# Optimization experiments

Hardware: AMD Instinct MI355X
Metric: run time of the kernel (lower is better)

The kernel has to match this reference:

```python
import jax, jax.numpy as jnp
import numpy as np

N = 100000   # nodes
E = 600000   # edges
IN = 12      # in_dim
H = 128      # hidden_dim
OUT = 2      # out_dim
L = 3        # num_layers
EPS = 1e-5   # BatchNorm eps


def setup_inputs() -> dict:
    key = jax.random.key(0)
    ks = jax.random.split(key, 14)
    s = 0.05
    return {
        "features": jax.random.normal(ks[0], (N, IN), jnp.float32),
        "edge_index": jax.random.randint(ks[1], (2, E), 0, N, dtype=jnp.int32).astype(jnp.int64),
        "emb_W": jax.random.normal(ks[2], (IN, H), jnp.float32) * s,
        "emb_b": jnp.zeros((H,), jnp.float32),
        "Wself": jax.random.normal(ks[3], (L, H, H), jnp.float32) * s,
        "Wneigh": jax.random.normal(ks[4], (L, H, H), jnp.float32) * s,
        "conv_b": jnp.zeros((L, H), jnp.float32),
        "bn_gamma": jnp.ones((L, H), jnp.float32),
        "bn_beta": jnp.zeros((L, H), jnp.float32),
        "W1": jax.random.normal(ks[5], (H, H // 2), jnp.float32) * s,
        "b1": jnp.zeros((H // 2,), jnp.float32),
        "W2": jax.random.normal(ks[6], (H // 2, OUT), jnp.float32) * s,
        "b2": jnp.zeros((OUT,), jnp.float32),
    }


def reference(features, edge_index, emb_W, emb_b, Wself, Wneigh, conv_b,
              bn_gamma, bn_beta, W1, b1, W2, b2):
    src, dst = edge_index[0], edge_index[1]
    # in-degree per destination node (loop-invariant)
    deg = jax.ops.segment_sum(jnp.ones((E,), features.dtype), dst, num_segments=N)
    inv_deg = 1.0 / jnp.maximum(deg, 1.0)  # [N]

    h = features @ emb_W + emb_b           # embedding: [N, H]
    h_last = h
    for i in range(L):
        # SAGEConv 'mean': gather src feats, scatter-sum to dst, divide by degree
        msg_sum = jax.ops.segment_sum(h[src], dst, num_segments=N)  # [N, H]
        h_neigh = msg_sum * inv_deg[:, None]
        h_new = h @ Wself[i] + h_neigh @ Wneigh[i] + conv_b[i]
        # BatchNorm1d over nodes (batch statistics)
        mu = jnp.mean(h_new, axis=0)
        var = jnp.var(h_new, axis=0)
        h_new = (h_new - mu) * jax.lax.rsqrt(var + EPS) * bn_gamma[i] + bn_beta[i]
        h_new = jax.nn.relu(h_new)
        # dropout is identity at inference
        if i > 0:
            h_new = h_new + h_last  # residual
        h_last = h_new
        h = h_new
    # MLP head
    out = jax.nn.relu(h @ W1 + b1) @ W2 + b2  # [N, 2]
    return out
```

## Files before the change

kernel.cpp:

```cpp
#include <hip/hip_runtime.h>
#include <hip/hip_bf16.h>
#include <cstdint>

#define H 128
#define EPS 1e-5f
#define CAP 32
#define NB 16

typedef unsigned int uint;
typedef unsigned short ushort;
typedef short short8 __attribute__((ext_vector_type(8)));
typedef float f32x4 __attribute__((ext_vector_type(4)));

__device__ __forceinline__ ushort f2bf(float f) {
  uint u = __float_as_uint(f);
  u += 0x7fffu + ((u >> 16) & 1u);
  return (ushort)(u >> 16);
}
__device__ __forceinline__ float bflo(uint v) { return __uint_as_float(v << 16); }
__device__ __forceinline__ float bfhi(uint v) { return __uint_as_float(v & 0xffff0000u); }

__global__ __launch_bounds__(256) void k_init(const void* __restrict__ ei, int N,
                                              uint* __restrict__ cnt, int* __restrict__ flag,
                                              const float* __restrict__ F, const float* __restrict__ embW,
                                              const float* __restrict__ embB,
                                              ushort* __restrict__ bufA, ushort* __restrict__ bufB,
                                              const float* __restrict__ Wself, const float* __restrict__ Wneigh,
                                              const float* __restrict__ W1,
                                              ushort* __restrict__ Wsw, ushort* __restrict__ W1sw,
                                              float* __restrict__ bn_all,
                                              int ZB, int EB) {
  __shared__ float sW[12 * 128];
  __shared__ float sF[256 * 12];
  int b = blockIdx.x, t = threadIdx.x;
  if (b < ZB) {
    int i = b * 256 + t;
    if (i < N) cnt[i] = 0u;
    if (b == 0) {
      for (int j = t; j < NB * 256 * 3; j += 256) bn_all[j] = 0.f;
      if (t == 0) {
        const long long* p = (const long long*)ei;
        int ok = 1;
        for (int j = 0; j < 16; ++j) {
          long long s = p[j];
          if (s < 0 || s >= (long long)N) ok = 0;
        }
        *flag = ok;
      }
    }
    return;
  }
  if (b < ZB + EB) {
    int blk = b - ZB;
    for (int i = t; i < 12 * 128; i += 256) sW[i] = embW[i];
    int row0 = blk * 256;
    int nrows = min(256, N - row0);
    for (int i = t; i < nrows * 12; i += 256) sF[i] = F[(size_t)row0 * 12 + i];
    __syncthreads();
    int col = t & 127, half = t >> 7;
    float bias = embB[col];
    int rlo = half * 128, rhi = min(nrows, rlo + 128);
    for (int r = rlo; r < rhi; ++r) {
      float acc = bias;
#pragma unroll
      for (int k = 0; k < 12; ++k) acc = fmaf(sF[r * 12 + k], sW[k * 128 + col], acc);
      bufA[(size_t)(row0 + r) * H + col] = f2bf(acc);
    }
    if (blk == 0 && t < 128) {
      bufA[(size_t)N * H + t] = 0;
      bufB[(size_t)N * H + t] = 0;
    }
    return;
  }
  int e = (b - ZB - EB) * 256 + t;
  if (e < 3 * 4096) {
    int l = e >> 12, r = e & 4095;
    int kt = r >> 9, nt = (r >> 6) & 7, lane = r & 63;
    int quad = lane >> 4, l16 = lane & 15;
    int n = nt * 16 + l16;
    ushort* dst = Wsw + ((size_t)l * 4096 + (kt * 8 + nt) * 64 + lane) * 8;
#pragma unroll
    for (int j = 0; j < 8; ++j) {
      int k = kt * 32 + quad * 8 + j;
      float v = (k < 128) ? Wself[(size_t)l * H * H + (size_t)k * H + n]
                          : Wneigh[(size_t)l * H * H + (size_t)(k - 128) * H + n];
      dst[j] = f2bf(v);
    }
  } else if (e < 3 * 4096 + 1024) {
    int r = e - 3 * 4096;
    int kt = r >> 8, nt = (r >> 6) & 3, lane = r & 63;
    int quad = lane >> 4, l16 = lane & 15;
    int n = nt * 16 + l16;
    ushort* dst = W1sw + ((size_t)((kt * 4 + nt) * 64 + lane)) * 8;
#pragma unroll
    for (int j = 0; j < 8; ++j) {
      int k = kt * 32 + quad * 8 + j;
      dst[j] = f2bf(W1[(size_t)k * 64 + n]);
    }
  }
}

__global__ __launch_bounds__(256) void k_fill(const void* __restrict__ ei, uint* __restrict__ cnt,
                                              uint* __restrict__ csr, int E,
                                              const int* __restrict__ flag) {
  int e0 = (blockIdx.x * 256 + threadIdx.x) * 2;
  if (e0 >= E) return;
  int is64 = *flag;
  int s0, s1 = -1, d0, d1 = -1;
  bool two = (e0 + 1 < E);
  if (is64) {
    const unsigned long long* p = (const unsigned long long*)ei;
    if (two) {
      ulong2 sv = *(const ulong2*)(p + e0);
      ulong2 dv = *(const ulong2*)(p + E + e0);
      s0 = (int)sv.x; s1 = (int)sv.y; d0 = (int)dv.x; d1 = (int)dv.y;
    } else {
      s0 = (int)p[e0]; d0 = (int)p[E + e0];
    }
  } else {
    const int* p = (const int*)ei;
    if (two) {
      int2 sv = *(const int2*)(p + e0);
      int2 dv = *(const int2*)(p + E + e0);
      s0 = sv.x; s1 = sv.y; d0 = dv.x; d1 = dv.y;
    } else {
      s0 = p[e0]; d0 = p[E + e0];
    }
  }
  uint p0 = atomicAdd(&cnt[d0], 1u);
  if (p0 < (uint)CAP) csr[(size_t)d0 * CAP + p0] = (uint)s0;
  if (two) {
    uint p1 = atomicAdd(&cnt[d1], 1u);
    if (p1 < (uint)CAP) csr[(size_t)d1 * CAP + p1] = (uint)s1;
  }
}

__global__ __launch_bounds__(256, 4) void k_gg(const ushort* __restrict__ h, ushort* __restrict__ z,
                                               const uint* __restrict__ cnt, const uint* __restrict__ csr,
                                               const ushort* __restrict__ Wsw, const float* __restrict__ bias,
                                               float* __restrict__ bn_acc, int N) {
  __shared__ ushort sMsg[128 * 128];
  int tid = threadIdx.x;
  int wave = tid >> 6, lane = tid & 63, quad = lane >> 4, l16 = lane & 15;
  int row0 = blockIdx.x * 128;

  {
    const uint4* hu = (const uint4*)h;
#pragma unroll
    for (int p = 0; p < 8; ++p) {
      int nl = p * 16 + wave * 4 + quad;
      int n = row0 + nl;
      uint rawc = (n < N) ? cnt[n] : 0u;
      uint deg = min(rawc, (uint)CAP);
      const uint* row = csr + (size_t)n * CAP;
      float a0 = 0.f, a1 = 0.f, a2 = 0.f, a3 = 0.f, a4 = 0.f, a5 = 0.f, a6 = 0.f, a7 = 0.f;
      for (uint k = 0; k < deg; k += 8) {
        uint4 r0 = *(const uint4*)(row + k);
        uint4 r1 = *(const uint4*)(row + k + 4);
        uint raw[8] = {r0.x, r0.y, r0.z, r0.w, r1.x, r1.y, r1.z, r1.w};
        uint idx[8];
#pragma unroll
        for (int j = 0; j < 8; ++j) idx[j] = (k + j < deg) ? raw[j] : (uint)N;
        uint4 v[8];
#pragma unroll
        for (int j = 0; j < 8; ++j) v[j] = hu[(size_t)idx[j] * 16 + l16];
#pragma unroll
        for (int j = 0; j < 8; ++j) {
          a0 += bflo(v[j].x); a1 += bfhi(v[j].x);
          a2 += bflo(v[j].y); a3 += bfhi(v[j].y);
          a4 += bflo(v[j].z); a5 += bfhi(v[j].z);
          a6 += bflo(v[j].w); a7 += bfhi(v[j].w);
        }
      }
      float inv = 1.0f / (float)max(rawc, 1u);
      uint4 o;
      o.x = (uint)f2bf(a0 * inv) | ((uint)f2bf(a1 * inv) << 16);
      o.y = (uint)f2bf(a2 * inv) | ((uint)f2bf(a3 * inv) << 16);
      o.z = (uint)f2bf(a4 * inv) | ((uint)f2bf(a5 * inv) << 16);
      o.w = (uint)f2bf(a6 * inv) | ((uint)f2bf(a7 * inv) << 16);
      int off = nl * 256 + ((l16 * 16) ^ ((nl & 7) << 4));
      *(uint4*)((char*)sMsg + off) = o;
    }
  }

  int wrow0 = row0 + wave * 32;
  f32x4 acc[2][8];
#pragma unroll
  for (int m = 0; m < 2; ++m)
#pragma unroll
    for (int nt = 0; nt < 8; ++nt) acc[m][nt] = (f32x4){0.f, 0.f, 0.f, 0.f};
  short8 zf8 = {0, 0, 0, 0, 0, 0, 0, 0};
  const short8* Bp = (const short8*)Wsw;

#pragma unroll
  for (int kt = 0; kt < 4; ++kt) {
    int colb = kt * 32 + quad * 8;
    short8 a[2];
#pragma unroll
    for (int m = 0; m < 2; ++m) {
      int row = wrow0 + m * 16 + l16;
      a[m] = (row < N) ? *(const short8*)(h + (size_t)row * H + colb) : zf8;
    }
#pragma unroll
    for (int nt = 0; nt < 8; ++nt) {
      short8 bfr = Bp[(kt * 8 + nt) * 64 + lane];
#pragma unroll
      for (int m = 0; m < 2; ++m)
        acc[m][nt] = __builtin_amdgcn_mfma_f32_16x16x32_bf16(a[m], bfr, acc[m][nt], 0, 0, 0);
    }
  }
  __syncthreads();
#pragma unroll
  for (int kt = 4; kt < 8; ++kt) {
    int cb = (kt - 4) * 64 + quad * 16;
    short8 a[2];
#pragma unroll
    for (int m = 0; m < 2; ++m) {
      int rl = wave * 32 + m * 16 + l16;
      a[m] = *(const short8*)((const char*)sMsg + rl * 256 + (cb ^ ((l16 & 7) << 4)));
    }
#pragma unroll
    for (int nt = 0; nt < 8; ++nt) {
      short8 bfr = Bp[(kt * 8 + nt) * 64 + lane];
#pragma unroll
      for (int m = 0; m < 2; ++m)
        acc[m][nt] = __builtin_amdgcn_mfma_f32_16x16x32_bf16(a[m], bfr, acc[m][nt], 0, 0, 0);
    }
  }

  float bs[8];
#pragma unroll
  for (int nt = 0; nt < 8; ++nt) bs[nt] = bias[nt * 16 + l16];
  float ps[8], pq[8];
#pragma unroll
  for (int nt = 0; nt < 8; ++nt) { ps[nt] = 0.f; pq[nt] = 0.f; }
#pragma unroll
  for (int m = 0; m < 2; ++m) {
#pragma unroll
    for (int nt = 0; nt < 8; ++nt) {
      int col = nt * 16 + l16;
#pragma unroll
      for (int r = 0; r < 4; ++r) {
        int row = wrow0 + m * 16 + quad * 4 + r;
        if (row < N) {
          float v = acc[m][nt][r] + bs[nt];
          z[(size_t)row * H + col] = f2bf(v);
          ps[nt] += v; pq[nt] += v * v;
        }
      }
    }
  }
  __syncthreads();
  float* red = (float*)sMsg;
  int wq = wave * 4 + quad;
#pragma unroll
  for (int nt = 0; nt < 8; ++nt) {
    red[(wq * 8 + nt) * 17 + l16] = ps[nt];
    red[2176 + (wq * 8 + nt) * 17 + l16] = pq[nt];
  }
  __syncthreads();
  if (tid < 128) {
    int nt = tid >> 4, lc = tid & 15;
    float s = 0.f, q = 0.f;
#pragma unroll
    for (int w2i = 0; w2i < 16; ++w2i) {
      s += red[(w2i * 8 + nt) * 17 + lc];
      q += red[2176 + (w2i * 8 + nt) * 17 + lc];
    }
    float* bank = bn_acc + (size_t)(blockIdx.x & (NB - 1)) * 256;
    atomicAdd(&bank[tid], s);
    atomicAdd(&bank[128 + tid], q);
  }
}

__global__ __launch_bounds__(256) void k_norm(uint4* __restrict__ z, const uint4* __restrict__ hprev,
                                              const float* __restrict__ bn_acc,
                                              const float* __restrict__ gamma,
                                              const float* __restrict__ beta,
                                              int residual, int n4, float invN) {
  __shared__ float ssc[128], ssh[128];
  int t = threadIdx.x;
  if (t < 128) {
    float s = 0.f, q = 0.f;
#pragma unroll
    for (int b = 0; b < NB; ++b) {
      s += bn_acc[b * 256 + t];
      q += bn_acc[b * 256 + 128 + t];
    }
    float mu = s * invN;
    float var = fmaxf(q * invN - mu * mu, 0.f);
    float sc = gamma[t] * rsqrtf(var + EPS);
    ssc[t] = sc;
    ssh[t] = beta[t] - mu * sc;
  }
  __syncthreads();
  int idx = blockIdx.x * 256 + t;
  if (idx >= n4) return;
  int j = (idx & 15) * 8;
  uint4 v = z[idx];
  float x0 = fmaxf(fmaf(bflo(v.x), ssc[j + 0], ssh[j + 0]), 0.f);
  float x1 = fmaxf(fmaf(bfhi(v.x), ssc[j + 1], ssh[j + 1]), 0.f);
  float x2 = fmaxf(fmaf(bflo(v.y), ssc[j + 2], ssh[j + 2]), 0.f);
  float x3 = fmaxf(fmaf(bfhi(v.y), ssc[j + 3], ssh[j + 3]), 0.f);
  float x4 = fmaxf(fmaf(bflo(v.z), ssc[j + 4], ssh[j + 4]), 0.f);
  float x5 = fmaxf(fmaf(bfhi(v.z), ssc[j + 5], ssh[j + 5]), 0.f);
  float x6 = fmaxf(fmaf(bflo(v.w), ssc[j + 6], ssh[j + 6]), 0.f);
  float x7 = fmaxf(fmaf(bfhi(v.w), ssc[j + 7], ssh[j + 7]), 0.f);
  if (residual) {
    uint4 r = hprev[idx];
    x0 += bflo(r.x); x1 += bfhi(r.x); x2 += bflo(r.y); x3 += bfhi(r.y);
    x4 += bflo(r.z); x5 += bfhi(r.z); x6 += bflo(r.w); x7 += bfhi(r.w);
  }
  uint4 o;
  o.x = (uint)f2bf(x0) | ((uint)f2bf(x1) << 16);
  o.y = (uint)f2bf(x2) | ((uint)f2bf(x3) << 16);
  o.z = (uint)f2bf(x4) | ((uint)f2bf(x5) << 16);
  o.w = (uint)f2bf(x6) | ((uint)f2bf(x7) << 16);
  z[idx] = o;
}

__global__ __launch_bounds__(256) void k_head(const ushort* __restrict__ z, const ushort* __restrict__ hprev,
                                              const float* __restrict__ bn_acc,
                                              const float* __restrict__ gamma,
                                              const float* __restrict__ beta, float invN,
                                              const ushort* __restrict__ W1sw,
                                              const float* __restrict__ b1, const float* __restrict__ W2,
                                              const float* __restrict__ b2, float* __restrict__ out, int N) {
  __shared__ float ssc[128], ssh[128];
  int tid = threadIdx.x;
  if (tid < 128) {
    float s = 0.f, q = 0.f;
#pragma unroll
    for (int b = 0; b < NB; ++b) {
      s += bn_acc[b * 256 + tid];
      q += bn_acc[b * 256 + 128 + tid];
    }
    float mu = s * invN;
    float var = fmaxf(q * invN - mu * mu, 0.f);
    float sc = gamma[tid] * rsqrtf(var + EPS);
    ssc[tid] = sc;
    ssh[tid] = beta[tid] - mu * sc;
  }
  __syncthreads();
  int wave = tid >> 6, lane = tid & 63, quad = lane >> 4, l16 = lane & 15;
  int wrow0 = blockIdx.x * 64 + wave * 16;
  int am = wrow0 + l16;
  bool avalid = am < N;
  short8 af[4];
#pragma unroll
  for (int kt = 0; kt < 4; ++kt) {
    int c0 = kt * 32 + quad * 8;
    uint4 vz = avalid ? ((const uint4*)z)[(size_t)am * 16 + kt * 4 + quad] : make_uint4(0, 0, 0, 0);
    uint4 vr = avalid ? ((const uint4*)hprev)[(size_t)am * 16 + kt * 4 + quad] : make_uint4(0, 0, 0, 0);
    float x0 = fmaxf(fmaf(bflo(vz.x), ssc[c0 + 0], ssh[c0 + 0]), 0.f) + bflo(vr.x);
    float x1 = fmaxf(fmaf(bfhi(vz.x), ssc[c0 + 1], ssh[c0 + 1]), 0.f) + bfhi(vr.x);
    float x2 = fmaxf(fmaf(bflo(vz.y), ssc[c0 + 2], ssh[c0 + 2]), 0.f) + bflo(vr.y);
    float x3 = fmaxf(fmaf(bfhi(vz.y), ssc[c0 + 3], ssh[c0 + 3]), 0.f) + bfhi(vr.y);
    float x4 = fmaxf(fmaf(bflo(vz.z), ssc[c0 + 4], ssh[c0 + 4]), 0.f) + bflo(vr.z);
    float x5 = fmaxf(fmaf(bfhi(vz.z), ssc[c0 + 5], ssh[c0 + 5]), 0.f) + bfhi(vr.z);
    float x6 = fmaxf(fmaf(bflo(vz.w), ssc[c0 + 6], ssh[c0 + 6]), 0.f) + bflo(vr.w);
    float x7 = fmaxf(fmaf(bfhi(vz.w), ssc[c0 + 7], ssh[c0 + 7]), 0.f) + bfhi(vr.w);
    ushort u[8] = {f2bf(x0), f2bf(x1), f2bf(x2), f2bf(x3), f2bf(x4), f2bf(x5), f2bf(x6), f2bf(x7)};
    af[kt] = *(short8*)u;
  }
  const short8* Bp = (const short8*)W1sw;
  f32x4 acc[4];
#pragma unroll
  for (int nt = 0; nt < 4; ++nt) acc[nt] = (f32x4){0.f, 0.f, 0.f, 0.f};
#pragma unroll
  for (int kt = 0; kt < 4; ++kt) {
#pragma unroll
    for (int nt = 0; nt < 4; ++nt) {
      short8 bfr = Bp[(kt * 4 + nt) * 64 + lane];
      acc[nt] = __builtin_amdgcn_mfma_f32_16x16x32_bf16(af[kt], bfr, acc[nt], 0, 0, 0);
    }
  }
  float p0[4] = {0.f, 0.f, 0.f, 0.f}, p1[4] = {0.f, 0.f, 0.f, 0.f};
#pragma unroll
  for (int nt = 0; nt < 4; ++nt) {
    int c = nt * 16 + l16;
    float bc = b1[c], w20 = W2[c * 2], w21 = W2[c * 2 + 1];
#pragma unroll
    for (int r = 0; r < 4; ++r) {
      float v = fmaxf(acc[nt][r] + bc, 0.f);
      p0[r] = fmaf(v, w20, p0[r]);
      p1[r] = fmaf(v, w21, p1[r]);
    }
  }
#pragma unroll
  for (int m = 1; m < 16; m <<= 1) {
#pragma unroll
    for (int r = 0; r < 4; ++r) {
      p0[r] += __shfl_xor(p0[r], m);
      p1[r] += __shfl_xor(p1[r], m);
    }
  }
  if (l16 == 0) {
    float b20 = b2[0], b21 = b2[1];
#pragma unroll
    for (int r = 0; r < 4; ++r) {
      int row = wrow0 + quad * 4 + r;
      if (row < N) {
        float2 o = make_float2(p0[r] + b20, p1[r] + b21);
        *(float2*)(out + (size_t)row * 2) = o;
      }
    }
  }
}

extern "C" void kernel_launch(void* const* d_in, const int* in_sizes, int n_in,
                              void* d_out, int out_size, void* d_ws, size_t ws_size,
                              hipStream_t stream) {
  const float* features = (const float*)d_in[0];
  const void*  edges    = d_in[1];
  const float* emb_W    = (const float*)d_in[2];
  const float* emb_b    = (const float*)d_in[3];
  const float* Wself    = (const float*)d_in[4];
  const float* Wneigh   = (const float*)d_in[5];
  const float* conv_b   = (const float*)d_in[6];
  const float* bn_gamma = (const float*)d_in[7];
  const float* bn_beta  = (const float*)d_in[8];
  const float* W1       = (const float*)d_in[9];
  const float* b1       = (const float*)d_in[10];
  const float* W2       = (const float*)d_in[11];
  const float* b2       = (const float*)d_in[12];
  float* out = (float*)d_out;
  const int N = in_sizes[0] / 12;
  const int E = in_sizes[1] / 2;
  const float invN = 1.0f / (float)N;

  char* ws = (char*)d_ws;
  size_t off = 0;
  auto take = [&](size_t bytes) {
    char* p = ws + off;
    off = (off + bytes + 511) & ~(size_t)511;
    return p;
  };
  int*    flag   = (int*)take(4);
  uint*   cnt    = (uint*)take((size_t)N * 4);
  uint*   csr    = (uint*)take((size_t)N * CAP * 4);
  float*  bn_all = (float*)take(NB * 256 * 3 * 4);
  ushort* Wsw    = (ushort*)take(3 * 4096 * 8 * 2);
  ushort* W1sw   = (ushort*)take(1024 * 8 * 2);
  ushort* bufA   = (ushort*)take(((size_t)N + 1) * H * 2);
  ushort* bufB   = (ushort*)take(((size_t)N + 1) * H * 2);

  const int ZB = (N + 255) / 256;
  const int EB = (N + 255) / 256;
  const int PB = (3 * 4096 + 1024 + 255) / 256;
  const int FB = (E + 511) / 512;
  const int GB = (N + 127) / 128;

  k_init<<<ZB + EB + PB, 256, 0, stream>>>(edges, N, cnt, flag, features, emb_W, emb_b,
                                           bufA, bufB, Wself, Wneigh, W1, Wsw, W1sw, bn_all, ZB, EB);
  k_fill<<<FB, 256, 0, stream>>>(edges, cnt, csr, E, flag);

  ushort* hbuf = bufA;
  ushort* obuf = bufB;
  const int n4 = N * 16;
  for (int i = 0; i < 3; ++i) {
    float* bn_i = bn_all + (size_t)i * NB * 256;
    k_gg<<<GB, 256, 0, stream>>>(hbuf, obuf, cnt, csr, Wsw + (size_t)i * 4096 * 8,
                                 conv_b + (size_t)i * H, bn_i, N);
    if (i < 2) {
      k_norm<<<(n4 + 255) / 256, 256, 0, stream>>>((uint4*)obuf, (const uint4*)hbuf, bn_i,
                                                   bn_gamma + (size_t)i * H, bn_beta + (size_t)i * H,
                                                   (i > 0) ? 1 : 0, n4, invN);
      ushort* t = hbuf; hbuf = obuf; obuf = t;
    }
  }
  k_head<<<(N + 63) / 64, 256, 0, stream>>>(obuf, hbuf, bn_all + (size_t)2 * NB * 256,
                                            bn_gamma + 2 * H, bn_beta + 2 * H,
                                            invN, W1sw, b1, W2, b2, out, N);
}
```

Baseline: 309.7 us.

## Fuse layer-0 BatchNorm+ReLU into layer-1 gather-GEMM and merge norm passes

Removes the standalone normalization pass after layer 0. The layer-1 gather/GEMM kernel now applies the layer-0 BN scale/shift and ReLU on the fly, both to gathered neighbor rows (with a mask for padding) and to the self rows. A combined k_norm2 later writes normalized layer-1 output plus the normalized layer-0 residual. This saves one full read/write pass over the N×128 activation, at the cost of extra ALU work per gathered element inside the bandwidth-bound gather loop.

Result: no change. 308.7 us (-0.3%).

```diff
diff --git a/kernel.cpp b/kernel.cpp
--- a/kernel.cpp
+++ b/kernel.cpp
@@ -19,6 +19,9 @@
 }
 __device__ __forceinline__ float bflo(uint v) { return __uint_as_float(v << 16); }
 __device__ __forceinline__ float bfhi(uint v) { return __uint_as_float(v & 0xffff0000u); }
+__device__ __forceinline__ float nrm(float x, float sc, float sh) {
+  return fmaxf(fmaf(x, sc, sh), 0.f);
+}
 
 __global__ __launch_bounds__(256) void k_init(const void* __restrict__ ei, int N,
                                               uint* __restrict__ cnt, int* __restrict__ flag,
@@ -135,14 +138,41 @@
   }
 }
 
+template <int MODE>
 __global__ __launch_bounds__(256, 4) void k_gg(const ushort* __restrict__ h, ushort* __restrict__ z,
                                                const uint* __restrict__ cnt, const uint* __restrict__ csr,
                                                const ushort* __restrict__ Wsw, const float* __restrict__ bias,
-                                               float* __restrict__ bn_acc, int N) {
+                                               float* __restrict__ bn_acc, int N,
+                                               const float* __restrict__ bn_prev,
+                                               const float* __restrict__ gprev,
+                                               const float* __restrict__ bprev, float invN) {
   __shared__ ushort sMsg[128 * 128];
+  __shared__ float ssc[128], ssh[128];
   int tid = threadIdx.x;
   int wave = tid >> 6, lane = tid & 63, quad = lane >> 4, l16 = lane & 15;
   int row0 = blockIdx.x * 128;
+
+  if (MODE) {
+    if (tid < 128) {
+      float s = 0.f, q = 0.f;
+#pragma unroll
+      for (int b = 0; b < NB; ++b) {
+        s += bn_prev[b * 256 + tid];
+        q += bn_prev[b * 256 + 128 + tid];
+      }
+      float mu = s * invN;
+      float var = fmaxf(q * invN - mu * mu, 0.f);
+      float sc = gprev[tid] * rsqrtf(var + EPS);
+      ssc[tid] = sc;
+      ssh[tid] = bprev[tid] - mu * sc;
+    }
+    __syncthreads();
+  }
+  float sc8[8], sh8[8];
+  if (MODE) {
+#pragma unroll
+    for (int e = 0; e < 8; ++e) { sc8[e] = ssc[l16 * 8 + e]; sh8[e] = ssh[l16 * 8 + e]; }
+  }
 
   {
     const uint4* hu = (const uint4*)h;
@@ -159,17 +189,33 @@
         uint4 r1 = *(const uint4*)(row + k + 4);
         uint raw[8] = {r0.x, r0.y, r0.z, r0.w, r1.x, r1.y, r1.z, r1.w};
         uint idx[8];
-#pragma unroll
-        for (int j = 0; j < 8; ++j) idx[j] = (k + j < deg) ? raw[j] : (uint)N;
+        float msk[8];
+#pragma unroll
+        for (int j = 0; j < 8; ++j) {
+          bool in = (k + j < deg);
+          idx[j] = in ? raw[j] : (uint)N;
+          msk[j] = in ? 1.f : 0.f;
+        }
         uint4 v[8];
 #pragma unroll
         for (int j = 0; j < 8; ++j) v[j] = hu[(size_t)idx[j] * 16 + l16];
 #pragma unroll
         for (int j = 0; j < 8; ++j) {
-          a0 += bflo(v[j].x); a1 += bfhi(v[j].x);
-          a2 += bflo(v[j].y); a3 += bfhi(v[j].y);
-          a4 += bflo(v[j].z); a5 += bfhi(v[j].z);
-          a6 += bflo(v[j].w); a7 += bfhi(v[j].w);
+          if (MODE) {
+            a0 = fmaf(nrm(bflo(v[j].x), sc8[0], sh8[0]), msk[j], a0);
+            a1 = fmaf(nrm(bfhi(v[j].x), sc8[1], sh8[1]), msk[j], a1);
+            a2 = fmaf(nrm(bflo(v[j].y), sc8[2], sh8[2]), msk[j], a2);
+            a3 = fmaf(nrm(bfhi(v[j].y), sc8[3], sh8[3]), msk[j], a3);
+            a4 = fmaf(nrm(bflo(v[j].z), sc8[4], sh8[4]), msk[j], a4);
+            a5 = fmaf(nrm(bfhi(v[j].z), sc8[5], sh8[5]), msk[j], a5);
+            a6 = fmaf(nrm(bflo(v[j].w), sc8[6], sh8[6]), msk[j], a6);
+            a7 = fmaf(nrm(bfhi(v[j].w), sc8[7], sh8[7]), msk[j], a7);
+          } else {
+            a0 += bflo(v[j].x); a1 += bfhi(v[j].x);
+            a2 += bflo(v[j].y); a3 += bfhi(v[j].y);
+            a4 += bflo(v[j].z); a5 += bfhi(v[j].z);
+            a6 += bflo(v[j].w); a7 += bfhi(v[j].w);
+          }
         }
       }
       float inv = 1.0f / (float)max(rawc, 1u);
@@ -195,11 +241,34 @@
 #pragma unroll
   for (int kt = 0; kt < 4; ++kt) {
     int colb = kt * 32 + quad * 8;
+    float scv[8], shv[8];
+    if (MODE) {
+#pragma unroll
+      for (int e = 0; e < 8; ++e) { scv[e] = ssc[colb + e]; shv[e] = ssh[colb + e]; }
+    }
     short8 a[2];
 #pragma unroll
     for (int m = 0; m < 2; ++m) {
       int row = wrow0 + m * 16 + l16;
-      a[m] = (row < N) ? *(const short8*)(h + (size_t)row * H + colb) : zf8;
+      if (row < N) {
+        if (MODE) {
+          uint4 vz = *(const uint4*)(h + (size_t)row * H + colb);
+          ushort u[8];
+          u[0] = f2bf(nrm(bflo(vz.x), scv[0], shv[0]));
+          u[1] = f2bf(nrm(bfhi(vz.x), scv[1], shv[1]));
+          u[2] = f2bf(nrm(bflo(vz.y), scv[2], shv[2]));
+          u[3] = f2bf(nrm(bfhi(vz.y), scv[3], shv[3]));
+          u[4] = f2bf(nrm(bflo(vz.z), scv[4], shv[4]));
+          u[5] = f2bf(nrm(bfhi(vz.z), scv[5], shv[5]));
+          u[6] = f2bf(nrm(bflo(vz.w), scv[6], shv[6]));
+          u[7] = f2bf(nrm(bfhi(vz.w), scv[7], shv[7]));
+          a[m] = *(short8*)u;
+        } else {
+          a[m] = *(const short8*)(h + (size_t)row * H + colb);
+        }
+      } else {
+        a[m] = zf8;
+      }
     }
 #pragma unroll
     for (int nt = 0; nt < 8; ++nt) {
@@ -273,50 +342,50 @@
   }
 }
 
-__global__ __launch_bounds__(256) void k_norm(uint4* __restrict__ z, const uint4* __restrict__ hprev,
-                                              const float* __restrict__ bn_acc,
-                                              const float* __restrict__ gamma,
-                                              const float* __restrict__ beta,
-                                              int residual, int n4, float invN) {
-  __shared__ float ssc[128], ssh[128];
+__global__ __launch_bounds__(256) void k_norm2(const uint4* __restrict__ z1, uint4* __restrict__ zh,
+                                               const float* __restrict__ bn1, const float* __restrict__ g1v,
+                                               const float* __restrict__ b1v,
+                                               const float* __restrict__ bn0, const float* __restrict__ g0v,
+                                               const float* __restrict__ b0v,
+                                               int n4, float invN) {
+  __shared__ float s1c[128], s1h[128], s0c[128], s0h[128];
   int t = threadIdx.x;
   if (t < 128) {
     float s = 0.f, q = 0.f;
 #pragma unroll
-    for (int b = 0; b < NB; ++b) {
-      s += bn_acc[b * 256 + t];
-      q += bn_acc[b * 256 + 128 + t];
-    }
+    for (int b = 0; b < NB; ++b) { s += bn1[b * 256 + t]; q += bn1[b * 256 + 128 + t]; }
     float mu = s * invN;
     float var = fmaxf(q * invN - mu * mu, 0.f);
-    float sc = gamma[t] * rsqrtf(var + EPS);
-    ssc[t] = sc;
-    ssh[t] = beta[t] - mu * sc;
+    float sc = g1v[t] * rsqrtf(var + EPS);
+    s1c[t] = sc; s1h[t] = b1v[t] - mu * sc;
+    s = 0.f; q = 0.f;
+#pragma unroll
+    for (int b = 0; b < NB; ++b) { s += bn0[b * 256 + t]; q += bn0[b * 256 + 128 + t]; }
+    mu = s * invN;
+    var = fmaxf(q * invN - mu * mu, 0.f);
+    sc = g0v[t] * rsqrtf(var + EPS);
+    s0c[t] = sc; s0h[t] = b0v[t] - mu * sc;
   }
   __syncthreads();
   int idx = blockIdx.x * 256 + t;
   if (idx >= n4) return;
   int j = (idx & 15) * 8;
-  uint4 v = z[idx];
-  float x0 = fmaxf(fmaf(bflo(v.x), ssc[j + 0], ssh[j + 0]), 0.f);
-  float x1 = fmaxf(fmaf(bfhi(v.x), ssc[j + 1], ssh[j + 1]), 0.f);
-  float x2 = fmaxf(fmaf(bflo(v.y), ssc[j + 2], ssh[j + 2]), 0.f);
-  float x3 = fmaxf(fmaf(bfhi(v.y), ssc[j + 3], ssh[j + 3]), 0.f);
-  float x4 = fmaxf(fmaf(bflo(v.z), ssc[j + 4], ssh[j + 4]), 0.f);
-  float x5 = fmaxf(fmaf(bfhi(v.z), ssc[j + 5], ssh[j + 5]), 0.f);
-  float x6 = fmaxf(fmaf(bflo(v.w), ssc[j + 6], ssh[j + 6]), 0.f);
-  float x7 = fmaxf(fmaf(bfhi(v.w), ssc[j + 7], ssh[j + 7]), 0.f);
-  if (residual) {
-    uint4 r = hprev[idx];
-    x0 += bflo(r.x); x1 += bfhi(r.x); x2 += bflo(r.y); x3 += bfhi(r.y);
-    x4 += bflo(r.z); x5 += bfhi(r.z); x6 += bflo(r.w); x7 += bfhi(r.w);
-  }
+  uint4 v = z1[idx];
+  uint4 r = zh[idx];
+  float x0 = nrm(bflo(v.x), s1c[j + 0], s1h[j + 0]) + nrm(bflo(r.x), s0c[j + 0], s0h[j + 0]);
+  float x1 = nrm(bfhi(v.x), s1c[j + 1], s1h[j + 1]) + nrm(bfhi(r.x), s0c[j + 1], s0h[j + 1]);
+  float x2 = nrm(bflo(v.y), s1c[j + 2], s1h[j + 2]) + nrm(bflo(r.y), s0c[j + 2], s0h[j + 2]);
+  float x3 = nrm(bfhi(v.y), s1c[j + 3], s1h[j + 3]) + nrm(bfhi(r.y), s0c[j + 3], s0h[j + 3]);
+  float x4 = nrm(bflo(v.z), s1c[j + 4], s1h[j + 4]) + nrm(bflo(r.z), s0c[j + 4], s0h[j + 4]);
+  float x5 = nrm(bfhi(v.z), s1c[j + 5], s1h[j + 5]) + nrm(bfhi(r.z), s0c[j + 5], s0h[j + 5]);
+  float x6 = nrm(bflo(v.w), s1c[j + 6], s1h[j + 6]) + nrm(bflo(r.w), s0c[j + 6], s0h[j + 6]);
+  float x7 = nrm(bfhi(v.w), s1c[j + 7], s1h[j + 7]) + nrm(bfhi(r.w), s0c[j + 7], s0h[j + 7]);
   uint4 o;
   o.x = (uint)f2bf(x0) | ((uint)f2bf(x1) << 16);
   o.y = (uint)f2bf(x2) | ((uint)f2bf(x3) << 16);
   o.z = (uint)f2bf(x4) | ((uint)f2bf(x5) << 16);
   o.w = (uint)f2bf(x6) | ((uint)f2bf(x7) << 16);
-  z[idx] = o;
+  zh[idx] = o;
 }
 
 __global__ __launch_bounds__(256) void k_head(const ushort* __restrict__ z, const ushort* __restrict__ hprev,
@@ -352,14 +421,14 @@
     int c0 = kt * 32 + quad * 8;
     uint4 vz = avalid ? ((const uint4*)z)[(size_t)am * 16 + kt * 4 + quad] : make_uint4(0, 0, 0, 0);
     uint4 vr = avalid ? ((const uint4*)hprev)[(size_t)am * 16 + kt * 4 + quad] : make_uint4(0, 0, 0, 0);
-    float x0 = fmaxf(fmaf(bflo(vz.x), ssc[c0 + 0], ssh[c0 + 0]), 0.f) + bflo(vr.x);
-    float x1 = fmaxf(fmaf(bfhi(vz.x), ssc[c0 + 1], ssh[c0 + 1]), 0.f) + bfhi(vr.x);
-    float x2 = fmaxf(fmaf(bflo(vz.y), ssc[c0 + 2], ssh[c0 + 2]), 0.f) + bflo(vr.y);
-    float x3 = fmaxf(fmaf(bfhi(vz.y), ssc[c0 + 3], ssh[c0 + 3]), 0.f) + bfhi(vr.y);
-    float x4 = fmaxf(fmaf(bflo(vz.z), ssc[c0 + 4], ssh[c0 + 4]), 0.f) + bflo(vr.z);
-    float x5 = fmaxf(fmaf(bfhi(vz.z), ssc[c0 + 5], ssh[c0 + 5]), 0.f) + bfhi(vr.z);
-    float x6 = fmaxf(fmaf(bflo(vz.w), ssc[c0 + 6], ssh[c0 + 6]), 0.f) + bflo(vr.w);
-    float x7 = fmaxf(fmaf(bfhi(vz.w), ssc[c0 + 7], ssh[c0 + 7]), 0.f) + bfhi(vr.w);
+    float x0 = nrm(bflo(vz.x), ssc[c0 + 0], ssh[c0 + 0]) + bflo(vr.x);
+    float x1 = nrm(bfhi(vz.x), ssc[c0 + 1], ssh[c0 + 1]) + bfhi(vr.x);
+    float x2 = nrm(bflo(vz.y), ssc[c0 + 2], ssh[c0 + 2]) + bflo(vr.y);
+    float x3 = nrm(bfhi(vz.y), ssc[c0 + 3], ssh[c0 + 3]) + bfhi(vr.y);
+    float x4 = nrm(bflo(vz.z), ssc[c0 + 4], ssh[c0 + 4]) + bflo(vr.z);
+    float x5 = nrm(bfhi(vz.z), ssc[c0 + 5], ssh[c0 + 5]) + bfhi(vr.z);
+    float x6 = nrm(bflo(vz.w), ssc[c0 + 6], ssh[c0 + 6]) + bflo(vr.w);
+    float x7 = nrm(bfhi(vz.w), ssc[c0 + 7], ssh[c0 + 7]) + bfhi(vr.w);
     ushort u[8] = {f2bf(x0), f2bf(x1), f2bf(x2), f2bf(x3), f2bf(x4), f2bf(x5), f2bf(x6), f2bf(x7)};
     af[kt] = *(short8*)u;
   }
@@ -455,21 +524,20 @@
                                            bufA, bufB, Wself, Wneigh, W1, Wsw, W1sw, bn_all, ZB, EB);
   k_fill<<<FB, 256, 0, stream>>>(edges, cnt, csr, E, flag);
 
-  ushort* hbuf = bufA;
-  ushort* obuf = bufB;
+  float* bn0 = bn_all;
+  float* bn1 = bn_all + (size_t)NB * 256;
+  float* bn2 = bn_all + (size_t)2 * NB * 256;
   const int n4 = N * 16;
-  for (int i = 0; i < 3; ++i) {
-    float* bn_i = bn_all + (size_t)i * NB * 256;
-    k_gg<<<GB, 256, 0, stream>>>(hbuf, obuf, cnt, csr, Wsw + (size_t)i * 4096 * 8,
-                                 conv_b + (size_t)i * H, bn_i, N);
-    if (i < 2) {
-      k_norm<<<(n4 + 255) / 256, 256, 0, stream>>>((uint4*)obuf, (const uint4*)hbuf, bn_i,
-                                                   bn_gamma + (size_t)i * H, bn_beta + (size_t)i * H,
-                                                   (i > 0) ? 1 : 0, n4, invN);
-      ushort* t = hbuf; hbuf = obuf; obuf = t;
-    }
-  }
-  k_head<<<(N + 63) / 64, 256, 0, stream>>>(obuf, hbuf, bn_all + (size_t)2 * NB * 256,
-                                            bn_gamma + 2 * H, bn_beta + 2 * H,
+
+  k_gg<0><<<GB, 256, 0, stream>>>(bufA, bufB, cnt, csr, Wsw, conv_b, bn0, N,
+                                  nullptr, nullptr, nullptr, invN);
+  k_gg<1><<<GB, 256, 0, stream>>>(bufB, bufA, cnt, csr, Wsw + (size_t)4096 * 8, conv_b + H, bn1, N,
+                                  bn0, bn_gamma, bn_beta, invN);
+  k_norm2<<<(n4 + 255) / 256, 256, 0, stream>>>((const uint4*)bufA, (uint4*)bufB,
+                                                bn1, bn_gamma + H, bn_beta + H,
+                                                bn0, bn_gamma, bn_beta, n4, invN);
+  k_gg<0><<<GB, 256, 0, stream>>>(bufB, bufA, cnt, csr, Wsw + (size_t)2 * 4096 * 8, conv_b + 2 * H,
+                                  bn2, N, nullptr, nullptr, nullptr, invN);
+  k_head<<<(N + 63) / 64, 256, 0, stream>>>(bufA, bufB, bn2, bn_gamma + 2 * H, bn_beta + 2 * H,
                                             invN, W1sw, b1, W2, b2, out, N);
 }
```

## Fuse BatchNorm apply into layer kernel via grid barrier, merge CSR fill

Applied to the files above, without the earlier changes.

For layers 0 and 1, the conv/GEMM kernel now keeps its pre-norm results in registers. It waits at a grid-wide atomic barrier until all blocks have contributed batch statistics, then computes scale and shift and writes the normalized ReLU (plus residual) output directly. This removes two separate normalize passes over the N×128 bf16 activations and their launches. Separately, the zero-init work moves into its own small kernel so the edge CSR fill can share one launch with the embedding and weight packing. The barrier relies on all blocks being co-resident, so it is only used when the grid has at most 1024 blocks; blocks spin-wait while stragglers finish.

Measured after the change: 650.6 us. 2.1x slower.

```diff
diff --git a/kernel.cpp b/kernel.cpp
--- a/kernel.cpp
+++ b/kernel.cpp
@@ -19,39 +19,82 @@
 }
 __device__ __forceinline__ float bflo(uint v) { return __uint_as_float(v << 16); }
 __device__ __forceinline__ float bfhi(uint v) { return __uint_as_float(v & 0xffff0000u); }
-
-__global__ __launch_bounds__(256) void k_init(const void* __restrict__ ei, int N,
+__device__ __forceinline__ float nrm(float x, float sc, float sh) {
+  return fmaxf(fmaf(x, sc, sh), 0.f);
+}
+
+__global__ __launch_bounds__(256) void k_zero(const void* __restrict__ ei, int N,
                                               uint* __restrict__ cnt, int* __restrict__ flag,
+                                              float* __restrict__ bn_all, uint* __restrict__ bar,
+                                              ushort* __restrict__ bufA, ushort* __restrict__ bufB) {
+  int b = blockIdx.x, t = threadIdx.x;
+  int i = b * 256 + t;
+  if (i < N) cnt[i] = 0u;
+  if (b == 0) {
+    for (int j = t; j < NB * 256 * 3; j += 256) bn_all[j] = 0.f;
+    if (t < 2) bar[t] = 0u;
+    if (t < 128) {
+      bufA[(size_t)N * H + t] = 0;
+      bufB[(size_t)N * H + t] = 0;
+    }
+    if (t == 0) {
+      const long long* p = (const long long*)ei;
+      int ok = 1;
+      for (int j = 0; j < 16; ++j) {
+        long long s = p[j];
+        if (s < 0 || s >= (long long)N) ok = 0;
+      }
+      *flag = ok;
+    }
+  }
+}
+
+__global__ __launch_bounds__(256) void k_work(const void* __restrict__ ei, uint* __restrict__ cnt,
+                                              uint* __restrict__ csr, int E, const int* __restrict__ flag,
                                               const float* __restrict__ F, const float* __restrict__ embW,
-                                              const float* __restrict__ embB,
-                                              ushort* __restrict__ bufA, ushort* __restrict__ bufB,
+                                              const float* __restrict__ embB, ushort* __restrict__ bufA,
                                               const float* __restrict__ Wself, const float* __restrict__ Wneigh,
                                               const float* __restrict__ W1,
                                               ushort* __restrict__ Wsw, ushort* __restrict__ W1sw,
-                                              float* __restrict__ bn_all,
-                                              int ZB, int EB) {
+                                              int N, int FB, int EB) {
   __shared__ float sW[12 * 128];
   __shared__ float sF[256 * 12];
   int b = blockIdx.x, t = threadIdx.x;
-  if (b < ZB) {
-    int i = b * 256 + t;
-    if (i < N) cnt[i] = 0u;
-    if (b == 0) {
-      for (int j = t; j < NB * 256 * 3; j += 256) bn_all[j] = 0.f;
-      if (t == 0) {
-        const long long* p = (const long long*)ei;
-        int ok = 1;
-        for (int j = 0; j < 16; ++j) {
-          long long s = p[j];
-          if (s < 0 || s >= (long long)N) ok = 0;
-        }
-        *flag = ok;
-      }
+  if (b < FB) {
+    int e0 = (b * 256 + t) * 2;
+    if (e0 >= E) return;
+    int is64 = *flag;
+    int s0, s1 = -1, d0, d1 = -1;
+    bool two = (e0 + 1 < E);
+    if (is64) {
+      const unsigned long long* p = (const unsigned long long*)ei;
+      if (two) {
+        ulong2 sv = *(const ulong2*)(p + e0);
+        ulong2 dv = *(const ulong2*)(p + E + e0);
+        s0 = (int)sv.x; s1 = (int)sv.y; d0 = (int)dv.x; d1 = (int)dv.y;
+      } else {
+        s0 = (int)p[e0]; d0 = (int)p[E + e0];
+      }
+    } else {
+      const int* p = (const int*)ei;
+      if (two) {
+        int2 sv = *(const int2*)(p + e0);
+        int2 dv = *(const int2*)(p + E + e0);
+        s0 = sv.x; s1 = sv.y; d0 = dv.x; d1 = dv.y;
+      } else {
+        s0 = p[e0]; d0 = p[E + e0];
+      }
+    }
+    uint p0 = atomicAdd(&cnt[d0], 1u);
+    if (p0 < (uint)CAP) csr[(size_t)d0 * CAP + p0] = (uint)s0;
+    if (two) {
+      uint p1 = atomicAdd(&cnt[d1], 1u);
+      if (p1 < (uint)CAP) csr[(size_t)d1 * CAP + p1] = (uint)s1;
     }
     return;
   }
-  if (b < ZB + EB) {
-    int blk = b - ZB;
+  if (b < FB + EB) {
+    int blk = b - FB;
     for (int i = t; i < 12 * 128; i += 256) sW[i] = embW[i];
     int row0 = blk * 256;
     int nrows = min(256, N - row0);
@@ -66,13 +109,9 @@
       for (int k = 0; k < 12; ++k) acc = fmaf(sF[r * 12 + k], sW[k * 128 + col], acc);
       bufA[(size_t)(row0 + r) * H + col] = f2bf(acc);
     }
-    if (blk == 0 && t < 128) {
-      bufA[(size_t)N * H + t] = 0;
-      bufB[(size_t)N * H + t] = 0;
-    }
     return;
   }
-  int e = (b - ZB - EB) * 256 + t;
+  int e = (b - FB - EB) * 256 + t;
   if (e < 3 * 4096) {
     int l = e >> 12, r = e & 4095;
     int kt = r >> 9, nt = (r >> 6) & 7, lane = r & 63;
@@ -100,46 +139,15 @@
   }
 }
 
-__global__ __launch_bounds__(256) void k_fill(const void* __restrict__ ei, uint* __restrict__ cnt,
-                                              uint* __restrict__ csr, int E,
-                                              const int* __restrict__ flag) {
-  int e0 = (blockIdx.x * 256 + threadIdx.x) * 2;
-  if (e0 >= E) return;
-  int is64 = *flag;
-  int s0, s1 = -1, d0, d1 = -1;
-  bool two = (e0 + 1 < E);
-  if (is64) {
-    const unsigned long long* p = (const unsigned long long*)ei;
-    if (two) {
-      ulong2 sv = *(const ulong2*)(p + e0);
-      ulong2 dv = *(const ulong2*)(p + E + e0);
-      s0 = (int)sv.x; s1 = (int)sv.y; d0 = (int)dv.x; d1 = (int)dv.y;
-    } else {
-      s0 = (int)p[e0]; d0 = (int)p[E + e0];
-    }
-  } else {
-    const int* p = (const int*)ei;
-    if (two) {
-      int2 sv = *(const int2*)(p + e0);
-      int2 dv = *(const int2*)(p + E + e0);
-      s0 = sv.x; s1 = sv.y; d0 = dv.x; d1 = dv.y;
-    } else {
-      s0 = p[e0]; d0 = p[E + e0];
-    }
-  }
-  uint p0 = atomicAdd(&cnt[d0], 1u);
-  if (p0 < (uint)CAP) csr[(size_t)d0 * CAP + p0] = (uint)s0;
-  if (two) {
-    uint p1 = atomicAdd(&cnt[d1], 1u);
-    if (p1 < (uint)CAP) csr[(size_t)d1 * CAP + p1] = (uint)s1;
-  }
-}
-
-__global__ __launch_bounds__(256, 4) void k_gg(const ushort* __restrict__ h, ushort* __restrict__ z,
-                                               const uint* __restrict__ cnt, const uint* __restrict__ csr,
-                                               const ushort* __restrict__ Wsw, const float* __restrict__ bias,
-                                               float* __restrict__ bn_acc, int N) {
+template <int RES, int FUSE>
+__global__ __launch_bounds__(256, 4) void k_layer(const ushort* __restrict__ h, ushort* __restrict__ hout,
+                                                  const uint* __restrict__ cnt, const uint* __restrict__ csr,
+                                                  const ushort* __restrict__ Wsw, const float* __restrict__ bias,
+                                                  float* __restrict__ bn_acc, uint* __restrict__ bar, int N,
+                                                  const float* __restrict__ gamma, const float* __restrict__ beta,
+                                                  float invN) {
   __shared__ ushort sMsg[128 * 128];
+  __shared__ float ssc[128], ssh[128];
   int tid = threadIdx.x;
   int wave = tid >> 6, lane = tid & 63, quad = lane >> 4, l16 = lane & 15;
   int row0 = blockIdx.x * 128;
@@ -244,7 +252,8 @@
         int row = wrow0 + m * 16 + quad * 4 + r;
         if (row < N) {
           float v = acc[m][nt][r] + bs[nt];
-          z[(size_t)row * H + col] = f2bf(v);
+          acc[m][nt][r] = v;
+          if (!FUSE) hout[(size_t)row * H + col] = f2bf(v);
           ps[nt] += v; pq[nt] += v * v;
         }
       }
@@ -270,6 +279,49 @@
     float* bank = bn_acc + (size_t)(blockIdx.x & (NB - 1)) * 256;
     atomicAdd(&bank[tid], s);
     atomicAdd(&bank[128 + tid], q);
+  }
+  if (!FUSE) return;
+
+  __syncthreads();
+  if (tid == 0) {
+    __threadfence();
+    atomicAdd(bar, 1u);
+    while (__hip_atomic_load(bar, __ATOMIC_ACQUIRE, __HIP_MEMORY_SCOPE_AGENT) < gridDim.x)
+      __builtin_amdgcn_s_sleep(1);
+  }
+  __syncthreads();
+
+  if (tid < 128) {
+    float s = 0.f, q = 0.f;
+#pragma unroll
+    for (int b = 0; b < NB; ++b) {
+      s += __hip_atomic_load(&bn_acc[b * 256 + tid], __ATOMIC_RELAXED, __HIP_MEMORY_SCOPE_AGENT);
+      q += __hip_atomic_load(&bn_acc[b * 256 + 128 + tid], __ATOMIC_RELAXED, __HIP_MEMORY_SCOPE_AGENT);
+    }
+    float mu = s * invN;
+    float var = fmaxf(q * invN - mu * mu, 0.f);
+    float sc = gamma[tid] * rsqrtf(var + EPS);
+    ssc[tid] = sc;
+    ssh[tid] = beta[tid] - mu * sc;
+  }
+  __syncthreads();
+
+#pragma unroll
+  for (int m = 0; m < 2; ++m) {
+#pragma unroll
+    for (int nt = 0; nt < 8; ++nt) {
+      int col = nt * 16 + l16;
+      float sc = ssc[col], sh = ssh[col];
+#pragma unroll
+      for (int r = 0; r < 4; ++r) {
+        int row = wrow0 + m * 16 + quad * 4 + r;
+        if (row < N) {
+          float x = nrm(acc[m][nt][r], sc, sh);
+          if (RES) x += __uint_as_float(((uint)h[(size_t)row * H + col]) << 16);
+          hout[(size_t)row * H + col] = f2bf(x);
+        }
+      }
+    }
   }
 }
 
@@ -298,14 +350,14 @@
   if (idx >= n4) return;
   int j = (idx & 15) * 8;
   uint4 v = z[idx];
-  float x0 = fmaxf(fmaf(bflo(v.x), ssc[j + 0], ssh[j + 0]), 0.f);
-  float x1 = fmaxf(fmaf(bfhi(v.x), ssc[j + 1], ssh[j + 1]), 0.f);
-  float x2 = fmaxf(fmaf(bflo(v.y), ssc[j + 2], ssh[j + 2]), 0.f);
-  float x3 = fmaxf(fmaf(bfhi(v.y), ssc[j + 3], ssh[j + 3]), 0.f);
-  float x4 = fmaxf(fmaf(bflo(v.z), ssc[j + 4], ssh[j + 4]), 0.f);
-  float x5 = fmaxf(fmaf(bfhi(v.z), ssc[j + 5], ssh[j + 5]), 0.f);
-  float x6 = fmaxf(fmaf(bflo(v.w), ssc[j + 6], ssh[j + 6]), 0.f);
-  float x7 = fmaxf(fmaf(bfhi(v.w), ssc[j + 7], ssh[j + 7]), 0.f);
+  float x0 = nrm(bflo(v.x), ssc[j + 0], ssh[j + 0]);
+  float x1 = nrm(bfhi(v.x), ssc[j + 1], ssh[j + 1]);
+  float x2 = nrm(bflo(v.y), ssc[j + 2], ssh[j + 2]);
+  float x3 = nrm(bfhi(v.y), ssc[j + 3], ssh[j + 3]);
+  float x4 = nrm(bflo(v.z), ssc[j + 4], ssh[j + 4]);
+  float x5 = nrm(bfhi(v.z), ssc[j + 5], ssh[j + 5]);
+  float x6 = nrm(bflo(v.w), ssc[j + 6], ssh[j + 6]);
+  float x7 = nrm(bfhi(v.w), ssc[j + 7], ssh[j + 7]);
   if (residual) {
     uint4 r = hprev[idx];
     x0 += bflo(r.x); x1 += bfhi(r.x); x2 += bflo(r.y); x3 += bfhi(r.y);
@@ -352,14 +404,14 @@
     int c0 = kt * 32 + quad * 8;
     uint4 vz = avalid ? ((const uint4*)z)[(size_t)am * 16 + kt * 4 + quad] : make_uint4(0, 0, 0, 0);
     uint4 vr = avalid ? ((const uint4*)hprev)[(size_t)am * 16 + kt * 4 + quad] : make_uint4(0, 0, 0, 0);
-    float x0 = fmaxf(fmaf(bflo(vz.x), ssc[c0 + 0], ssh[c0 + 0]), 0.f) + bflo(vr.x);
-    float x1 = fmaxf(fmaf(bfhi(vz.x), ssc[c0 + 1], ssh[c0 + 1]), 0.f) + bfhi(vr.x);
-    float x2 = fmaxf(fmaf(bflo(vz.y), ssc[c0 + 2], ssh[c0 + 2]), 0.f) + bflo(vr.y);
-    float x3 = fmaxf(fmaf(bfhi(vz.y), ssc[c0 + 3], ssh[c0 + 3]), 0.f) + bfhi(vr.y);
-    float x4 = fmaxf(fmaf(bflo(vz.z), ssc[c0 + 4], ssh[c0 + 4]), 0.f) + bflo(vr.z);
-    float x5 = fmaxf(fmaf(bfhi(vz.z), ssc[c0 + 5], ssh[c0 + 5]), 0.f) + bfhi(vr.z);
-    float x6 = fmaxf(fmaf(bflo(vz.w), ssc[c0 + 6], ssh[c0 + 6]), 0.f) + bflo(vr.w);
-    float x7 = fmaxf(fmaf(bfhi(vz.w), ssc[c0 + 7], ssh[c0 + 7]), 0.f) + bfhi(vr.w);
+    float x0 = nrm(bflo(vz.x), ssc[c0 + 0], ssh[c0 + 0]) + bflo(vr.x);
+    float x1 = nrm(bfhi(vz.x), ssc[c0 + 1], ssh[c0 + 1]) + bfhi(vr.x);
+    float x2 = nrm(bflo(vz.y), ssc[c0 + 2], ssh[c0 + 2]) + bflo(vr.y);
+    float x3 = nrm(bfhi(vz.y), ssc[c0 + 3], ssh[c0 + 3]) + bfhi(vr.y);
+    float x4 = nrm(bflo(vz.z), ssc[c0 + 4], ssh[c0 + 4]) + bflo(vr.z);
+    float x5 = nrm(bfhi(vz.z), ssc[c0 + 5], ssh[c0 + 5]) + bfhi(vr.z);
+    float x6 = nrm(bflo(vz.w), ssc[c0 + 6], ssh[c0 + 6]) + bflo(vr.w);
+    float x7 = nrm(bfhi(vz.w), ssc[c0 + 7], ssh[c0 + 7]) + bfhi(vr.w);
     ushort u[8] = {f2bf(x0), f2bf(x1), f2bf(x2), f2bf(x3), f2bf(x4), f2bf(x5), f2bf(x6), f2bf(x7)};
     af[kt] = *(short8*)u;
   }
@@ -437,6 +489,7 @@
     return p;
   };
   int*    flag   = (int*)take(4);
+  uint*   bar    = (uint*)take(8);
   uint*   cnt    = (uint*)take((size_t)N * 4);
   uint*   csr    = (uint*)take((size_t)N * CAP * 4);
   float*  bn_all = (float*)take(NB * 256 * 3 * 4);
@@ -451,25 +504,38 @@
   const int FB = (E + 511) / 512;
   const int GB = (N + 127) / 128;
 
-  k_init<<<ZB + EB + PB, 256, 0, stream>>>(edges, N, cnt, flag, features, emb_W, emb_b,
-                                           bufA, bufB, Wself, Wneigh, W1, Wsw, W1sw, bn_all, ZB, EB);
-  k_fill<<<FB, 256, 0, stream>>>(edges, cnt, csr, E, flag);
-
-  ushort* hbuf = bufA;
-  ushort* obuf = bufB;
+  float* bn0 = bn_all;
+  float* bn1 = bn_all + (size_t)NB * 256;
+  float* bn2 = bn_all + (size_t)2 * NB * 256;
   const int n4 = N * 16;
-  for (int i = 0; i < 3; ++i) {
-    float* bn_i = bn_all + (size_t)i * NB * 256;
-    k_gg<<<GB, 256, 0, stream>>>(hbuf, obuf, cnt, csr, Wsw + (size_t)i * 4096 * 8,
-                                 conv_b + (size_t)i * H, bn_i, N);
-    if (i < 2) {
-      k_norm<<<(n4 + 255) / 256, 256, 0, stream>>>((uint4*)obuf, (const uint4*)hbuf, bn_i,
-                                                   bn_gamma + (size_t)i * H, bn_beta + (size_t)i * H,
-                                                   (i > 0) ? 1 : 0, n4, invN);
-      ushort* t = hbuf; hbuf = obuf; obuf = t;
-    }
-  }
-  k_head<<<(N + 63) / 64, 256, 0, stream>>>(obuf, hbuf, bn_all + (size_t)2 * NB * 256,
-                                            bn_gamma + 2 * H, bn_beta + 2 * H,
-                                            invN, W1sw, b1, W2, b2, out, N);
-}
+
+  k_zero<<<ZB, 256, 0, stream>>>(edges, N, cnt, flag, bn_all, bar, bufA, bufB);
+  k_work<<<FB + EB + PB, 256, 0, stream>>>(edges, cnt, csr, E, flag, features, emb_W, emb_b,
+                                           bufA, Wself, Wneigh, W1, Wsw, W1sw, N, FB, EB);
+
+  if (GB <= 1024) {
+    k_layer<0, 1><<<GB, 256, 0, stream>>>(bufA, bufB, cnt, csr, Wsw, conv_b, bn0, bar, N,
+                                          bn_gamma, bn_beta, invN);
+    k_layer<1, 1><<<GB, 256, 0, stream>>>(bufB, bufA, cnt, csr, Wsw + (size_t)4096 * 8,
+                                          conv_b + H, bn1, bar + 1, N,
+                                          bn_gamma + H, bn_beta + H, invN);
+    k_layer<0, 0><<<GB, 256, 0, stream>>>(bufA, bufB, cnt, csr, Wsw + (size_t)2 * 4096 * 8,
+                                          conv_b + 2 * H, bn2, nullptr, N,
+                                          nullptr, nullptr, invN);
+    k_head<<<(N + 63) / 64, 256, 0, stream>>>(bufB, bufA, bn2, bn_gamma + 2 * H, bn_beta + 2 * H,
+                                              invN, W1sw, b1, W2, b2, out, N);
+  } else {
+    k_layer<0, 0><<<GB, 256, 0, stream>>>(bufA, bufB, cnt, csr, Wsw, conv_b, bn0, nullptr, N,
+                                          nullptr, nullptr, invN);
+    k_norm<<<(n4 + 255) / 256, 256, 0, stream>>>((uint4*)bufB, nullptr, bn0,
+                                                 bn_gamma, bn_beta, 0, n4, invN);
+    k_layer<0, 0><<<GB, 256, 0, stream>>>(bufB, bufA, cnt, csr, Wsw + (size_t)4096 * 8,
+                                          conv_b + H, bn1, nullptr, N, nullptr, nullptr, invN);
+    k_norm<<<(n4 + 255) / 256, 256, 0, stream>>>((uint4*)bufA, (const uint4*)bufB, bn1,
+                                                 bn_gamma + H, bn_beta + H, 1, n4, invN);
+    k_layer<0, 0><<<GB, 256, 0, stream>>>(bufA, bufB, cnt, csr, Wsw + (size_t)2 * 4096 * 8,
+                                          conv_b + 2 * H, bn2, nullptr, N, nullptr, nullptr, invN);
+    k_head<<<(N + 63) / 64, 256, 0, stream>>>(bufB, bufA, bn2, bn_gamma + 2 * H, bn_beta + 2 * H,
+                                              invN, W1sw, b1, W2, b2, out, N);
+  }
+}
```
